# Kernel tuning notes

Hardware: AMD Instinct MI355X
Metric: run time of the kernel (lower is better)

The kernel has to match this reference:

```python
import jax, jax.numpy as jnp
import numpy as np

E = 16        # ensemble size
D_IN = 512    # input_dim
H = 512       # hidden width (hidden=[512,512])
D_OUT = 1     # output_dim
B = 8192      # batch


def _xavier(key, shape, fan_in, fan_out):
    # Xavier/Glorot uniform, matching layer_init='Xavier'
    limit = np.sqrt(6.0 / (fan_in + fan_out)).astype(np.float32)
    return jax.random.uniform(key, shape, jnp.float32, -limit, limit)


def setup_inputs() -> dict:
    key = jax.random.key(0)
    ks = jax.random.split(key, 7)
    x = jax.random.normal(ks[0], (B, D_IN), dtype=jnp.float32)
    # stacked per-ensemble-member weights (equivalent to E independent MLPs)
    W1 = _xavier(ks[1], (E, D_IN, H), D_IN, H)
    b1 = jnp.zeros((E, H), dtype=jnp.float32)
    W2 = _xavier(ks[2], (E, H, H), H, H)
    b2 = jnp.zeros((E, H), dtype=jnp.float32)
    W3 = _xavier(ks[3], (E, H, D_OUT), H, D_OUT)
    b3 = jnp.zeros((E, D_OUT), dtype=jnp.float32)
    return {"x": x, "W1": W1, "b1": b1, "W2": W2, "b2": b2, "W3": W3, "b3": b3}


def reference(x, W1, b1, W2, b2, W3, b3):
    # Batched over the ensemble dim: one grouped GEMM per layer instead of E small ones.
    h1 = jax.nn.relu(jnp.einsum('bi,eih->ebh', x, W1) + b1[:, None, :])   # [E,B,H]
    h2 = jax.nn.relu(jnp.einsum('ebh,ehk->ebk', h1, W2) + b2[:, None, :])  # [E,B,H]
    out = jnp.einsum('ebh,eho->ebo', h2, W3) + b3[:, None, :]              # [E,B,D_OUT]
    return out
```

## Files before the change

kernel.cpp:

```cpp
#include <hip/hip_runtime.h>


#define E_N   16
#define DIN   512
#define HID   512
#define BATCH 8192
#define BT    64
#define NBT   (BATCH / BT)
#define NBLK  (E_N * NBT)

typedef __attribute__((ext_vector_type(8))) short bf16x8;
typedef __attribute__((ext_vector_type(4))) float f32x4;

#define IMG_BYTES   131072
#define XPACK_BYTES ((size_t)NBT * IMG_BYTES)
#define WP_PER_E    (32 * 16 * 2048)
#define WP_BYTES    ((size_t)E_N * WP_PER_E)

__device__ __forceinline__ short f2bf(float f) {
  unsigned u = __builtin_bit_cast(unsigned, f);
  u += 0x7fffu + ((u >> 16) & 1u);
  return (short)(u >> 16);
}
__device__ __forceinline__ float bf2f(short s) {
  unsigned u = ((unsigned)(unsigned short)s) << 16;
  return __builtin_bit_cast(float, u);
}

__global__ void pack_x_kernel(const float* __restrict__ x, char* __restrict__ xp) {
  int t  = blockIdx.x * blockDim.x + threadIdx.x;
  int b  = t >> 6;
  int c8 = (t & 63) << 3;
  const float* src = x + (size_t)b * DIN + c8;
  bf16x8 hi, lo;
#pragma unroll
  for (int j = 0; j < 8; ++j) {
    float v = src[j];
    short h = f2bf(v);
    hi[j] = h;
    lo[j] = f2bf(v - bf2f(h));
  }
  int btile = b >> 6, r = b & 63;
  char* img = xp + (size_t)btile * IMG_BYTES;
  int inrow = (c8 << 1) ^ ((r & 15) << 4);
  *(bf16x8*)(img + (r << 10) + inrow) = hi;
  *(bf16x8*)(img + 65536 + (r << 10) + inrow) = lo;
}

__global__ void pack_w_kernel(const float* __restrict__ w, char* __restrict__ wp) {
  int t    = blockIdx.x * blockDim.x + threadIdx.x;
  int lane = t & 63;
  int kb   = (t >> 6) & 15;
  int nt   = (t >> 10) & 31;
  int e    = t >> 15;
  int k0 = kb * 32 + (lane >> 4) * 8;
  int n  = nt * 16 + (lane & 15);
  const float* src = w + ((size_t)e * DIN + k0) * HID + n;
  bf16x8 hi, lo;
#pragma unroll
  for (int j = 0; j < 8; ++j) {
    float v = src[(size_t)j * HID];
    short h = f2bf(v);
    hi[j] = h;
    lo[j] = f2bf(v - bf2f(h));
  }
  char* dst = wp + ((size_t)((e * 32 + nt) * 16 + kb) << 11) + (lane << 4);
  *(bf16x8*)dst = hi;
  *(bf16x8*)(dst + 1024) = lo;
}

#define MFMA16(A, B, C) __builtin_amdgcn_mfma_f32_16x16x32_bf16(A, B, C, 0, 0, 0)

#define LOADB(dst, kb_) do {                                          \
    const int _k = (kb_) << 11;                                       \
    dst[0] = *(const bf16x8*)(w0 + _k);                               \
    dst[1] = *(const bf16x8*)(w0 + _k + 1024);                        \
    dst[2] = *(const bf16x8*)(w1 + _k);                               \
    dst[3] = *(const bf16x8*)(w1 + _k + 1024);                        \
  } while (0)

__global__ __launch_bounds__(1024, 1) void fused_mlp_kernel(
    const char* __restrict__ xp,
    const char* __restrict__ wp1,
    const char* __restrict__ wp2,
    const float* __restrict__ b1,
    const float* __restrict__ b2,
    const float* __restrict__ w3,
    const float* __restrict__ b3,
    float* __restrict__ out)
{
  __shared__ __align__(16) char lds[IMG_BYTES];
  __shared__ float out_acc[BT];

  const int tid    = threadIdx.x;
  const int lane   = tid & 63;
  const int wid    = tid >> 6;
  const int lane15 = lane & 15;
  const int h4     = (lane >> 4) << 4;
  const int aswz   = lane15 << 4;

  const int bid   = blockIdx.x;
  const int xcd   = bid & 7;
  const int slot  = bid >> 3;
  const int e     = (xcd << 1) | (slot >> 7);
  const int btile = slot & 127;

  {
    const char* src = xp + (size_t)btile * IMG_BYTES;
#pragma unroll
    for (int it = 0; it < 8; ++it) {
      int off = (it << 14) + (tid << 4);
      *(bf16x8*)(lds + off) = *(const bf16x8*)(src + off);
    }
  }
  if (tid < BT) out_acc[tid] = b3[e];

  int rb[4];
#pragma unroll
  for (int mt = 0; mt < 4; ++mt) rb[mt] = ((mt << 4) + lane15) << 10;

  float bias1[2], bias2[2], w3v[2];
#pragma unroll
  for (int ntl = 0; ntl < 2; ++ntl) {
    int c = wid * 32 + ntl * 16 + lane15;
    bias1[ntl] = b1[e * HID + c];
    bias2[ntl] = b2[e * HID + c];
    w3v[ntl]   = w3[e * HID + c];
  }

  const char* wA0 = wp1 + (size_t)e * WP_PER_E + ((size_t)(wid * 2 + 0) << 15) + (lane << 4);
  const char* wA1 = wp1 + (size_t)e * WP_PER_E + ((size_t)(wid * 2 + 1) << 15) + (lane << 4);
  const char* wB0 = wp2 + (size_t)e * WP_PER_E + ((size_t)(wid * 2 + 0) << 15) + (lane << 4);
  const char* wB1 = wp2 + (size_t)e * WP_PER_E + ((size_t)(wid * 2 + 1) << 15) + (lane << 4);

  __syncthreads();

  f32x4 acc[4][2];

  auto run_layer = [&](const char* w0, const char* w1) {
    bf16x8 Bb[2][4];
    LOADB(Bb[0], 0);
#pragma unroll
    for (int kb = 0; kb < 16; ++kb) {
      if (kb < 15) LOADB(Bb[(kb + 1) & 1], kb + 1);
      bf16x8 Ah[4], Al[4];
      const int ca = ((kb << 6) + h4) ^ aswz;
#pragma unroll
      for (int mt = 0; mt < 4; ++mt) {
        const char* pa = lds + rb[mt] + ca;
        Ah[mt] = *(const bf16x8*)pa;
        Al[mt] = *(const bf16x8*)(pa + 65536);
      }
#pragma unroll
      for (int mt = 0; mt < 4; ++mt)
#pragma unroll
        for (int ntl = 0; ntl < 2; ++ntl) {
          const bf16x8 bh = Bb[kb & 1][ntl * 2];
          const bf16x8 bl = Bb[kb & 1][ntl * 2 + 1];
          acc[mt][ntl] = MFMA16(Ah[mt], bh, acc[mt][ntl]);
          acc[mt][ntl] = MFMA16(Ah[mt], bl, acc[mt][ntl]);
          acc[mt][ntl] = MFMA16(Al[mt], bh, acc[mt][ntl]);
        }
    }
  };

#pragma unroll
  for (int mt = 0; mt < 4; ++mt)
#pragma unroll
    for (int ntl = 0; ntl < 2; ++ntl)
      acc[mt][ntl] = (f32x4){0.f, 0.f, 0.f, 0.f};

  run_layer(wA0, wA1);

  __syncthreads();

#pragma unroll
  for (int mt = 0; mt < 4; ++mt)
#pragma unroll
    for (int ntl = 0; ntl < 2; ++ntl) {
      const int C2 = (wid * 32 + ntl * 16 + lane15) << 1;
#pragma unroll
      for (int q = 0; q < 4; ++q) {
        const int R = mt * 16 + (lane >> 4) * 4 + q;
        float v = acc[mt][ntl][q] + bias1[ntl];
        v = fmaxf(v, 0.f);
        short hb = f2bf(v);
        short lb = f2bf(v - bf2f(hb));
        const int inrow = C2 ^ ((R & 15) << 4);
        *(short*)(lds + (R << 10) + inrow) = hb;
        *(short*)(lds + 65536 + (R << 10) + inrow) = lb;
      }
    }

  __syncthreads();

#pragma unroll
  for (int mt = 0; mt < 4; ++mt)
#pragma unroll
    for (int ntl = 0; ntl < 2; ++ntl)
      acc[mt][ntl] = (f32x4){0.f, 0.f, 0.f, 0.f};

  run_layer(wB0, wB1);

#pragma unroll
  for (int mt = 0; mt < 4; ++mt)
#pragma unroll
    for (int q = 0; q < 4; ++q) {
      float p = 0.f;
#pragma unroll
      for (int ntl = 0; ntl < 2; ++ntl)
        p += fmaxf(acc[mt][ntl][q] + bias2[ntl], 0.f) * w3v[ntl];
      p += __shfl_xor(p, 1);
      p += __shfl_xor(p, 2);
      p += __shfl_xor(p, 4);
      p += __shfl_xor(p, 8);
      if (lane15 == 0)
        atomicAdd(&out_acc[mt * 16 + (lane >> 4) * 4 + q], p);
    }

  __syncthreads();
  if (tid < BT)
    out[(size_t)e * BATCH + btile * BT + tid] = out_acc[tid];
}

extern "C" void kernel_launch(void* const* d_in, const int* in_sizes, int n_in,
                              void* d_out, int out_size, void* d_ws, size_t ws_size,
                              hipStream_t stream) {
  (void)in_sizes; (void)n_in; (void)out_size; (void)ws_size;
  const float* x  = (const float*)d_in[0];
  const float* W1 = (const float*)d_in[1];
  const float* b1 = (const float*)d_in[2];
  const float* W2 = (const float*)d_in[3];
  const float* b2 = (const float*)d_in[4];
  const float* W3 = (const float*)d_in[5];
  const float* b3 = (const float*)d_in[6];

  char* xp  = (char*)d_ws;
  char* wp1 = xp + XPACK_BYTES;
  char* wp2 = wp1 + WP_BYTES;

  pack_x_kernel<<<2048, 256, 0, stream>>>(x, xp);
  pack_w_kernel<<<2048, 256, 0, stream>>>(W1, wp1);
  pack_w_kernel<<<2048, 256, 0, stream>>>(W2, wp2);
  fused_mlp_kernel<<<NBLK, 1024, 0, stream>>>(xp, wp1, wp2, b1, b2, W3, b3,
                                              (float*)d_out);
}
```

Measured before the change: 483.1 us.

## Halve batch tile to 32 rows with 512-thread blocks, two blocks per CU

```diff
diff --git a/kernel.cpp b/kernel.cpp
--- a/kernel.cpp
+++ b/kernel.cpp
@@ -5,14 +5,15 @@
 #define DIN   512
 #define HID   512
 #define BATCH 8192
-#define BT    64
+#define BT    32
 #define NBT   (BATCH / BT)
 #define NBLK  (E_N * NBT)
 
 typedef __attribute__((ext_vector_type(8))) short bf16x8;
 typedef __attribute__((ext_vector_type(4))) float f32x4;
 
-#define IMG_BYTES   131072
+#define IMG_BYTES   65536
+#define PLANE       32768
 #define XPACK_BYTES ((size_t)NBT * IMG_BYTES)
 #define WP_PER_E    (32 * 16 * 2048)
 #define WP_BYTES    ((size_t)E_N * WP_PER_E)
@@ -40,11 +41,11 @@
     hi[j] = h;
     lo[j] = f2bf(v - bf2f(h));
   }
-  int btile = b >> 6, r = b & 63;
+  int btile = b >> 5, r = b & 31;
   char* img = xp + (size_t)btile * IMG_BYTES;
   int inrow = (c8 << 1) ^ ((r & 15) << 4);
   *(bf16x8*)(img + (r << 10) + inrow) = hi;
-  *(bf16x8*)(img + 65536 + (r << 10) + inrow) = lo;
+  *(bf16x8*)(img + PLANE + (r << 10) + inrow) = lo;
 }
 
 __global__ void pack_w_kernel(const float* __restrict__ w, char* __restrict__ wp) {
@@ -71,15 +72,19 @@
 
 #define MFMA16(A, B, C) __builtin_amdgcn_mfma_f32_16x16x32_bf16(A, B, C, 0, 0, 0)
 
-#define LOADB(dst, kb_) do {                                          \
-    const int _k = (kb_) << 11;                                       \
-    dst[0] = *(const bf16x8*)(w0 + _k);                               \
-    dst[1] = *(const bf16x8*)(w0 + _k + 1024);                        \
-    dst[2] = *(const bf16x8*)(w1 + _k);                               \
-    dst[3] = *(const bf16x8*)(w1 + _k + 1024);                        \
+#define LOADB(dst, wb, kb_) do {                                       \
+    const int _k = (kb_) << 11;                                        \
+    dst[0] = *(const bf16x8*)(wb + _k);                                \
+    dst[1] = *(const bf16x8*)(wb + _k + 1024);                         \
+    dst[2] = *(const bf16x8*)(wb + _k + 32768);                        \
+    dst[3] = *(const bf16x8*)(wb + _k + 32768 + 1024);                 \
+    dst[4] = *(const bf16x8*)(wb + _k + 65536);                        \
+    dst[5] = *(const bf16x8*)(wb + _k + 65536 + 1024);                 \
+    dst[6] = *(const bf16x8*)(wb + _k + 98304);                        \
+    dst[7] = *(const bf16x8*)(wb + _k + 98304 + 1024);                 \
   } while (0)
 
-__global__ __launch_bounds__(1024, 1) void fused_mlp_kernel(
+__global__ __launch_bounds__(512, 2) void fused_mlp_kernel(
     const char* __restrict__ xp,
     const char* __restrict__ wp1,
     const char* __restrict__ wp2,
@@ -102,61 +107,58 @@
   const int bid   = blockIdx.x;
   const int xcd   = bid & 7;
   const int slot  = bid >> 3;
-  const int e     = (xcd << 1) | (slot >> 7);
-  const int btile = slot & 127;
+  const int e     = (xcd << 1) | (slot >> 8);
+  const int btile = slot & 255;
 
   {
     const char* src = xp + (size_t)btile * IMG_BYTES;
 #pragma unroll
     for (int it = 0; it < 8; ++it) {
-      int off = (it << 14) + (tid << 4);
+      int off = (it << 13) + (tid << 4);
       *(bf16x8*)(lds + off) = *(const bf16x8*)(src + off);
     }
   }
   if (tid < BT) out_acc[tid] = b3[e];
 
-  int rb[4];
-#pragma unroll
-  for (int mt = 0; mt < 4; ++mt) rb[mt] = ((mt << 4) + lane15) << 10;
-
-  float bias1[2], bias2[2], w3v[2];
-#pragma unroll
-  for (int ntl = 0; ntl < 2; ++ntl) {
-    int c = wid * 32 + ntl * 16 + lane15;
+  int rb[2];
+#pragma unroll
+  for (int mt = 0; mt < 2; ++mt) rb[mt] = ((mt << 4) + lane15) << 10;
+
+  float bias1[4], bias2[4], w3v[4];
+#pragma unroll
+  for (int ntl = 0; ntl < 4; ++ntl) {
+    int c = wid * 64 + ntl * 16 + lane15;
     bias1[ntl] = b1[e * HID + c];
     bias2[ntl] = b2[e * HID + c];
     w3v[ntl]   = w3[e * HID + c];
   }
 
-  const char* wA0 = wp1 + (size_t)e * WP_PER_E + ((size_t)(wid * 2 + 0) << 15) + (lane << 4);
-  const char* wA1 = wp1 + (size_t)e * WP_PER_E + ((size_t)(wid * 2 + 1) << 15) + (lane << 4);
-  const char* wB0 = wp2 + (size_t)e * WP_PER_E + ((size_t)(wid * 2 + 0) << 15) + (lane << 4);
-  const char* wB1 = wp2 + (size_t)e * WP_PER_E + ((size_t)(wid * 2 + 1) << 15) + (lane << 4);
-
-  __syncthreads();
-
-  f32x4 acc[4][2];
-
-  auto run_layer = [&](const char* w0, const char* w1) {
-    bf16x8 Bb[2][4];
-    LOADB(Bb[0], 0);
+  const char* wA = wp1 + (size_t)e * WP_PER_E + ((size_t)(wid * 4) << 15) + (lane << 4);
+  const char* wB = wp2 + (size_t)e * WP_PER_E + ((size_t)(wid * 4) << 15) + (lane << 4);
+
+  __syncthreads();
+
+  f32x4 acc[2][4];
+
+  auto run_layer = [&](const char* wb) {
 #pragma unroll
     for (int kb = 0; kb < 16; ++kb) {
-      if (kb < 15) LOADB(Bb[(kb + 1) & 1], kb + 1);
-      bf16x8 Ah[4], Al[4];
+      bf16x8 Bb[8];
+      LOADB(Bb, wb, kb);
+      bf16x8 Ah[2], Al[2];
       const int ca = ((kb << 6) + h4) ^ aswz;
 #pragma unroll
-      for (int mt = 0; mt < 4; ++mt) {
+      for (int mt = 0; mt < 2; ++mt) {
         const char* pa = lds + rb[mt] + ca;
         Ah[mt] = *(const bf16x8*)pa;
-        Al[mt] = *(const bf16x8*)(pa + 65536);
+        Al[mt] = *(const bf16x8*)(pa + PLANE);
       }
 #pragma unroll
-      for (int mt = 0; mt < 4; ++mt)
-#pragma unroll
-        for (int ntl = 0; ntl < 2; ++ntl) {
-          const bf16x8 bh = Bb[kb & 1][ntl * 2];
-          const bf16x8 bl = Bb[kb & 1][ntl * 2 + 1];
+      for (int mt = 0; mt < 2; ++mt)
+#pragma unroll
+        for (int ntl = 0; ntl < 4; ++ntl) {
+          const bf16x8 bh = Bb[ntl * 2];
+          const bf16x8 bl = Bb[ntl * 2 + 1];
           acc[mt][ntl] = MFMA16(Ah[mt], bh, acc[mt][ntl]);
           acc[mt][ntl] = MFMA16(Ah[mt], bl, acc[mt][ntl]);
           acc[mt][ntl] = MFMA16(Al[mt], bh, acc[mt][ntl]);
@@ -165,20 +167,20 @@
   };
 
 #pragma unroll
-  for (int mt = 0; mt < 4; ++mt)
-#pragma unroll
-    for (int ntl = 0; ntl < 2; ++ntl)
+  for (int mt = 0; mt < 2; ++mt)
+#pragma unroll
+    for (int ntl = 0; ntl < 4; ++ntl)
       acc[mt][ntl] = (f32x4){0.f, 0.f, 0.f, 0.f};
 
-  run_layer(wA0, wA1);
-
-  __syncthreads();
-
-#pragma unroll
-  for (int mt = 0; mt < 4; ++mt)
-#pragma unroll
-    for (int ntl = 0; ntl < 2; ++ntl) {
-      const int C2 = (wid * 32 + ntl * 16 + lane15) << 1;
+  run_layer(wA);
+
+  __syncthreads();
+
+#pragma unroll
+  for (int mt = 0; mt < 2; ++mt)
+#pragma unroll
+    for (int ntl = 0; ntl < 4; ++ntl) {
+      const int C2 = (wid * 64 + ntl * 16 + lane15) << 1;
 #pragma unroll
       for (int q = 0; q < 4; ++q) {
         const int R = mt * 16 + (lane >> 4) * 4 + q;
@@ -188,27 +190,27 @@
         short lb = f2bf(v - bf2f(hb));
         const int inrow = C2 ^ ((R & 15) << 4);
         *(short*)(lds + (R << 10) + inrow) = hb;
-        *(short*)(lds + 65536 + (R << 10) + inrow) = lb;
+        *(short*)(lds + PLANE + (R << 10) + inrow) = lb;
       }
     }
 
   __syncthreads();
 
 #pragma unroll
-  for (int mt = 0; mt < 4; ++mt)
-#pragma unroll
-    for (int ntl = 0; ntl < 2; ++ntl)
+  for (int mt = 0; mt < 2; ++mt)
+#pragma unroll
+    for (int ntl = 0; ntl < 4; ++ntl)
       acc[mt][ntl] = (f32x4){0.f, 0.f, 0.f, 0.f};
 
-  run_layer(wB0, wB1);
-
-#pragma unroll
-  for (int mt = 0; mt < 4; ++mt)
+  run_layer(wB);
+
+#pragma unroll
+  for (int mt = 0; mt < 2; ++mt)
 #pragma unroll
     for (int q = 0; q < 4; ++q) {
       float p = 0.f;
 #pragma unroll
-      for (int ntl = 0; ntl < 2; ++ntl)
+      for (int ntl = 0; ntl < 4; ++ntl)
         p += fmaxf(acc[mt][ntl][q] + bias2[ntl], 0.f) * w3v[ntl];
       p += __shfl_xor(p, 1);
       p += __shfl_xor(p, 2);
@@ -242,6 +244,6 @@
   pack_x_kernel<<<2048, 256, 0, stream>>>(x, xp);
   pack_w_kernel<<<2048, 256, 0, stream>>>(W1, wp1);
   pack_w_kernel<<<2048, 256, 0, stream>>>(W2, wp2);
-  fused_mlp_kernel<<<NBLK, 1024, 0, stream>>>(xp, wp1, wp2, b1, b2, W3, b3,
-                                              (float*)d_out);
-}
+  fused_mlp_kernel<<<NBLK, 512, 0, stream>>>(xp, wp1, wp2, b1, b2, W3, b3,
+                                             (float*)d_out);
+}
```

Result: slower. 493.4 us (+2.1%).
